# Kernel optimization log

Measured on AMD Instinct MI355X. Metric: run time of the kernel, lower is better.

Reference implementation:

```python
import jax, jax.numpy as jnp
import numpy as np

EPS = 1e-6
N_HEADS = 16


def _stable_softmax(x):
    # max subtracted with stop_gradient (torch .detach()), clamp to [-50, 50], eps in denom
    x_max = jax.lax.stop_gradient(jnp.max(x, axis=-1, keepdims=True))
    exp_x = jnp.exp(jnp.clip(x - x_max, -50.0, 50.0))
    return exp_x / (jnp.sum(exp_x, axis=-1, keepdims=True) + EPS)


def setup_inputs() -> dict:
    key = jax.random.key(0)
    k1, k2, k3 = jax.random.split(key, 3)
    B, S, D = 2, 2048, 1024
    x = jax.random.normal(k1, (B, S, D), dtype=jnp.float32)
    Wqkv = jax.random.normal(k2, (3 * D, D), dtype=jnp.float32) * 0.02
    Wout = jax.random.normal(k3, (D, D), dtype=jnp.float32) * (0.02 / np.sqrt(2))
    return {"x": x, "Wqkv": Wqkv, "Wout": Wout}


def reference(x, Wqkv, Wout):
    B, S, D = x.shape
    H = N_HEADS
    Dh = D // H
    scale = 1.0 / np.sqrt(Dh)
    # qkv projection (torch Linear: x @ W.T), split into q,k,v -> (B,H,S,Dh)
    qkv = (x @ Wqkv.T).reshape(B, S, 3, H, Dh)
    qkv = jnp.transpose(qkv, (2, 0, 3, 1, 4))
    q, k, v = qkv[0], qkv[1], qkv[2]
    # chunked attention is mathematically identical to full attention here
    scores = jnp.einsum('bhqd,bhkd->bhqk', q, k) * scale
    attn = _stable_softmax(scores)
    out = jnp.einsum('bhqk,bhkd->bhqd', attn, v)  # (B,H,S,Dh)
    out = jnp.transpose(out, (0, 2, 1, 3)).reshape(B, S, D)
    return out @ Wout.T
```

## Files before the change

### kernel.cpp

```cpp
#include <hip/hip_runtime.h>
#include <hip/hip_bf16.h>
#include <stdint.h>

#define S_LEN   2048
#define D_MODEL 1024
#define NH      16
#define DH      64
#define BATCH   2
#define TOKENS  (BATCH * S_LEN)

typedef __bf16 bf16;
typedef __bf16 bf16x8 __attribute__((ext_vector_type(8)));
typedef __bf16 b16x4  __attribute__((ext_vector_type(4)));
typedef short  s16x4  __attribute__((ext_vector_type(4)));
typedef float  f32x4  __attribute__((ext_vector_type(4)));

__device__ __forceinline__ void async_lds16(const void* g, void* l) {
  __builtin_amdgcn_global_load_lds((__attribute__((address_space(1))) void*)g,
                                   (__attribute__((address_space(3))) void*)l,
                                   16, 0, 0);
}

__global__ __launch_bounds__(256) void convert_kernel(
    const float* __restrict__ src, bf16* __restrict__ dst, int n8) {
  const int i = blockIdx.x * 256 + threadIdx.x;
  if (i >= n8) return;
  const f32x4 a = *(const f32x4*)(src + (size_t)i * 8);
  const f32x4 b = *(const f32x4*)(src + (size_t)i * 8 + 4);
  bf16x8 o;
#pragma unroll
  for (int j = 0; j < 4; j++) { o[j] = (bf16)a[j]; o[j + 4] = (bf16)b[j]; }
  *(bf16x8*)(dst + (size_t)i * 8) = o;
}

#define BM 128
#define BN 128
#define BK 32

#define GEMM_CORE(APTR, BPTR, KDIM)                                              \
  __shared__ __align__(16) bf16 As[BM * BK];                                     \
  __shared__ __align__(16) bf16 Bs[BN * BK];                                     \
  const int tid  = threadIdx.x;                                                  \
  const int wave = tid >> 6, lane = tid & 63;                                    \
  const int quad = lane >> 4, l16 = lane & 15;                                   \
  const int m0 = blockIdx.y * BM;                                                \
  const int n0 = blockIdx.x * BN;                                                \
  const int wm = (wave >> 1) * 64, wn = (wave & 1) * 64;                         \
  f32x4 acc[4][4] = {};                                                          \
  const int c0 = tid, c1 = tid + 256;                                            \
  for (int k0 = 0; k0 < (KDIM); k0 += BK) {                                      \
    async_lds16((APTR) + (size_t)(m0 + (c0 >> 2)) * (KDIM) + k0 + (c0 & 3) * 8,  \
                As + c0 * 8);                                                    \
    async_lds16((APTR) + (size_t)(m0 + (c1 >> 2)) * (KDIM) + k0 + (c1 & 3) * 8,  \
                As + c1 * 8);                                                    \
    async_lds16((BPTR) + (size_t)(n0 + (c0 >> 2)) * (KDIM) + k0 + (c0 & 3) * 8,  \
                Bs + c0 * 8);                                                    \
    async_lds16((BPTR) + (size_t)(n0 + (c1 >> 2)) * (KDIM) + k0 + (c1 & 3) * 8,  \
                Bs + c1 * 8);                                                    \
    __syncthreads();                                                             \
    bf16x8 af[4], bfr[4];                                                        \
    _Pragma("unroll") for (int i = 0; i < 4; i++)                                \
        af[i] = *(const bf16x8*)(As + (wm + i * 16 + l16) * BK + quad * 8);      \
    _Pragma("unroll") for (int j = 0; j < 4; j++)                                \
        bfr[j] = *(const bf16x8*)(Bs + (wn + j * 16 + l16) * BK + quad * 8);     \
    _Pragma("unroll") for (int i = 0; i < 4; i++)                                \
      _Pragma("unroll") for (int j = 0; j < 4; j++)                              \
        acc[i][j] = __builtin_amdgcn_mfma_f32_16x16x32_bf16(af[i], bfr[j],       \
                                                            acc[i][j], 0, 0, 0); \
    __syncthreads();                                                             \
  }

__global__ __launch_bounds__(256) void gemm_qkv_kernel(
    const bf16* __restrict__ X, const bf16* __restrict__ W,
    bf16* __restrict__ Qo, bf16* __restrict__ Ko, bf16* __restrict__ VTo) {
  GEMM_CORE(X, W, D_MODEL)
  const int t = n0 >> 10;
#pragma unroll
  for (int i = 0; i < 4; i++) {
    const int rowb = m0 + wm + i * 16 + quad * 4;
    const int b = rowb >> 11, s0 = rowb & 2047;
#pragma unroll
    for (int j = 0; j < 4; j++) {
      const int col = n0 + wn + j * 16 + l16;
      const int h = (col >> 6) & 15, d = col & 63;
      if (t == 2) {
        b16x4 v4;
#pragma unroll
        for (int r = 0; r < 4; r++) v4[r] = (bf16)acc[i][j][r];
        *(b16x4*)(VTo + ((size_t)(b * NH + h) * DH + d) * S_LEN + s0) = v4;
      } else {
#pragma unroll
        for (int r = 0; r < 4; r++) {
          const float v = acc[i][j][r];
          if (t == 0)
            Qo[((size_t)(b * NH + h) * S_LEN + s0 + r) * DH + d] = (bf16)(v * 0.125f);
          else
            Ko[((size_t)(b * NH + h) * S_LEN + s0 + r) * DH + d] = (bf16)v;
        }
      }
    }
  }
}

__global__ __launch_bounds__(256) void gemm_out_kernel(
    const bf16* __restrict__ A, const bf16* __restrict__ W,
    float* __restrict__ Out) {
  GEMM_CORE(A, W, D_MODEL)
#pragma unroll
  for (int i = 0; i < 4; i++) {
    const int rowb = m0 + wm + i * 16 + quad * 4;
#pragma unroll
    for (int j = 0; j < 4; j++) {
      const int col = n0 + wn + j * 16 + l16;
#pragma unroll
      for (int r = 0; r < 4; r++)
        Out[(size_t)(rowb + r) * D_MODEL + col] = acc[i][j][r];
    }
  }
}

#define AKS 72
#define AVS 72

__device__ __forceinline__ f32x4 mfma16(s16x4 a, s16x4 b, f32x4 c) {
  return __builtin_amdgcn_mfma_f32_16x16x16bf16_1k(a, b, c, 0, 0, 0);
}

__global__ __launch_bounds__(256) void attn_kernel(
    const bf16* __restrict__ Q, const bf16* __restrict__ K,
    const bf16* __restrict__ VT, bf16* __restrict__ AO) {
  __shared__ __align__(16) bf16 Ks[64 * AKS];
  __shared__ __align__(16) bf16 Vs[64 * AVS];

  const int tid  = threadIdx.x;
  const int wave = tid >> 6, lane = tid & 63;
  const int quad = lane >> 4, l16 = lane & 15;
  const int qb = blockIdx.x & 15;
  const int bh = blockIdx.x >> 4;
  const bf16* qp = Q  + (size_t)bh * S_LEN * DH;
  const bf16* kp = K  + (size_t)bh * S_LEN * DH;
  const bf16* vp = VT + (size_t)bh * DH * S_LEN;
  const int qr0 = qb * 128 + wave * 32;

  bf16x8 aq[2][2];
#pragma unroll
  for (int u = 0; u < 2; u++) {
    aq[u][0] = *(const bf16x8*)(qp + (size_t)(qr0 + u * 16 + l16) * DH + quad * 8);
    aq[u][1] = *(const bf16x8*)(qp + (size_t)(qr0 + u * 16 + l16) * DH + 32 + quad * 8);
  }

  f32x4 oT[2][4] = {};
  float lsum[2] = {0.f, 0.f};

  const int c0 = tid, c1 = tid + 256;
  const int r0c = c0 >> 3, r1c = c1 >> 3, k0c = (c0 & 7) * 8, k1c = (c1 & 7) * 8;

  for (int kb = 0; kb < S_LEN / 64; kb++) {
    const bf16x8 kv0 = *(const bf16x8*)(kp + (size_t)(kb * 64 + r0c) * DH + k0c);
    const bf16x8 kv1 = *(const bf16x8*)(kp + (size_t)(kb * 64 + r1c) * DH + k1c);
    const bf16x8 vv0 = *(const bf16x8*)(vp + (size_t)r0c * S_LEN + kb * 64 + k0c);
    const bf16x8 vv1 = *(const bf16x8*)(vp + (size_t)r1c * S_LEN + kb * 64 + k1c);
    __syncthreads();
    *(bf16x8*)(Ks + r0c * AKS + k0c) = kv0;
    *(bf16x8*)(Ks + r1c * AKS + k1c) = kv1;
    *(bf16x8*)(Vs + r0c * AVS + k0c) = vv0;
    *(bf16x8*)(Vs + r1c * AVS + k1c) = vv1;
    __syncthreads();

#pragma unroll
    for (int t = 0; t < 4; t++) {
      const bf16x8 ak0 = *(const bf16x8*)(Ks + (t * 16 + l16) * AKS + quad * 8);
      const bf16x8 ak1 = *(const bf16x8*)(Ks + (t * 16 + l16) * AKS + 32 + quad * 8);
      s16x4 av[4];
#pragma unroll
      for (int nt = 0; nt < 4; nt++)
        av[nt] = __builtin_bit_cast(
            s16x4, *(const b16x4*)(Vs + (nt * 16 + l16) * AVS + t * 16 + quad * 4));
#pragma unroll
      for (int u = 0; u < 2; u++) {
        f32x4 st = {};
        st = __builtin_amdgcn_mfma_f32_16x16x32_bf16(ak0, aq[u][0], st, 0, 0, 0);
        st = __builtin_amdgcn_mfma_f32_16x16x32_bf16(ak1, aq[u][1], st, 0, 0, 0);
        b16x4 pb;
#pragma unroll
        for (int r = 0; r < 4; r++) {
          pb[r] = (bf16)__expf(st[r]);
          lsum[u] += (float)pb[r];
        }
        const s16x4 pbs = __builtin_bit_cast(s16x4, pb);
#pragma unroll
        for (int nt = 0; nt < 4; nt++) oT[u][nt] = mfma16(av[nt], pbs, oT[u][nt]);
      }
    }
  }

#pragma unroll
  for (int u = 0; u < 2; u++) {
    float s = lsum[u];
    s += __shfl_xor(s, 16);
    s += __shfl_xor(s, 32);
    lsum[u] = s;
  }

  const int b = bh >> 4, h = bh & 15;
#pragma unroll
  for (int u = 0; u < 2; u++) {
    const float inv = 1.0f / (lsum[u] + 1e-6f);
    const int srow = qr0 + u * 16 + l16;
    const size_t base = (size_t)(b * S_LEN + srow) * D_MODEL + h * DH;
#pragma unroll
    for (int nt = 0; nt < 4; nt++) {
      b16x4 o4;
#pragma unroll
      for (int r = 0; r < 4; r++) o4[r] = (bf16)(oT[u][nt][r] * inv);
      *(b16x4*)(AO + base + nt * 16 + quad * 4) = o4;
    }
  }
}

extern "C" void kernel_launch(void* const* d_in, const int* in_sizes, int n_in,
                              void* d_out, int out_size, void* d_ws, size_t ws_size,
                              hipStream_t stream) {
  const float* x    = (const float*)d_in[0];
  const float* wqkv = (const float*)d_in[1];
  const float* wout = (const float*)d_in[2];
  float* out = (float*)d_out;

  bf16* Q  = (bf16*)d_ws;
  bf16* K  = Q  + (size_t)TOKENS * D_MODEL;
  bf16* VT = K  + (size_t)TOKENS * D_MODEL;
  bf16* xb = VT + (size_t)TOKENS * D_MODEL;
  bf16* AO = xb;
  bf16* wqkvb = (bf16*)d_out;
  bf16* woutb = Q;

  convert_kernel<<<dim3(TOKENS * D_MODEL / (256 * 8)), dim3(256), 0, stream>>>(
      x, xb, TOKENS * D_MODEL / 8);
  convert_kernel<<<dim3(3 * D_MODEL * D_MODEL / (256 * 8)), dim3(256), 0, stream>>>(
      wqkv, wqkvb, 3 * D_MODEL * D_MODEL / 8);

  gemm_qkv_kernel<<<dim3(3 * D_MODEL / BN, TOKENS / BM), dim3(256), 0, stream>>>(
      xb, wqkvb, Q, K, VT);

  attn_kernel<<<dim3(BATCH * NH * (S_LEN / 128)), dim3(256), 0, stream>>>(Q, K, VT, AO);

  convert_kernel<<<dim3(D_MODEL * D_MODEL / (256 * 8)), dim3(256), 0, stream>>>(
      wout, woutb, D_MODEL * D_MODEL / 8);

  gemm_out_kernel<<<dim3(D_MODEL / BN, TOKENS / BM), dim3(256), 0, stream>>>(
      AO, woutb, out);
}
```

Baseline: 206.2 us.

## Stage P through LDS to use 16x16x32 MFMA for PV and prefetch K/V

The attention kernel now writes the bf16 probability tiles to a per-wave LDS buffer so the P·V product can use the wider 16x16x32 bf16 MFMA instead of the 16x16x16 variant, halving the PV MFMA count. It also software-prefetches the next K/V tile into registers while the current tile is computed, hiding global load latency. The row sum is now accumulated from the fp32 exponentials rather than the rounded bf16 values. This adds LDS traffic, extra LDS use per block, and register pressure from the prefetched tiles.

```diff
diff --git a/kernel.cpp b/kernel.cpp
--- a/kernel.cpp
+++ b/kernel.cpp
@@ -12,7 +12,6 @@
 typedef __bf16 bf16;
 typedef __bf16 bf16x8 __attribute__((ext_vector_type(8)));
 typedef __bf16 b16x4  __attribute__((ext_vector_type(4)));
-typedef short  s16x4  __attribute__((ext_vector_type(4)));
 typedef float  f32x4  __attribute__((ext_vector_type(4)));
 
 __device__ __forceinline__ void async_lds16(const void* g, void* l) {
@@ -121,16 +120,14 @@
 
 #define AKS 72
 #define AVS 72
-
-__device__ __forceinline__ f32x4 mfma16(s16x4 a, s16x4 b, f32x4 c) {
-  return __builtin_amdgcn_mfma_f32_16x16x16bf16_1k(a, b, c, 0, 0, 0);
-}
+#define PTS 72
 
 __global__ __launch_bounds__(256) void attn_kernel(
     const bf16* __restrict__ Q, const bf16* __restrict__ K,
     const bf16* __restrict__ VT, bf16* __restrict__ AO) {
   __shared__ __align__(16) bf16 Ks[64 * AKS];
   __shared__ __align__(16) bf16 Vs[64 * AVS];
+  __shared__ __align__(16) bf16 PT[4 * 32 * PTS];
 
   const int tid  = threadIdx.x;
   const int wave = tid >> 6, lane = tid & 63;
@@ -151,15 +148,17 @@
 
   f32x4 oT[2][4] = {};
   float lsum[2] = {0.f, 0.f};
+  bf16* PTw = PT + wave * (32 * PTS);
 
   const int c0 = tid, c1 = tid + 256;
   const int r0c = c0 >> 3, r1c = c1 >> 3, k0c = (c0 & 7) * 8, k1c = (c1 & 7) * 8;
 
+  bf16x8 kv0 = *(const bf16x8*)(kp + (size_t)r0c * DH + k0c);
+  bf16x8 kv1 = *(const bf16x8*)(kp + (size_t)r1c * DH + k1c);
+  bf16x8 vv0 = *(const bf16x8*)(vp + (size_t)r0c * S_LEN + k0c);
+  bf16x8 vv1 = *(const bf16x8*)(vp + (size_t)r1c * S_LEN + k1c);
+
   for (int kb = 0; kb < S_LEN / 64; kb++) {
-    const bf16x8 kv0 = *(const bf16x8*)(kp + (size_t)(kb * 64 + r0c) * DH + k0c);
-    const bf16x8 kv1 = *(const bf16x8*)(kp + (size_t)(kb * 64 + r1c) * DH + k1c);
-    const bf16x8 vv0 = *(const bf16x8*)(vp + (size_t)r0c * S_LEN + kb * 64 + k0c);
-    const bf16x8 vv1 = *(const bf16x8*)(vp + (size_t)r1c * S_LEN + kb * 64 + k1c);
     __syncthreads();
     *(bf16x8*)(Ks + r0c * AKS + k0c) = kv0;
     *(bf16x8*)(Ks + r1c * AKS + k1c) = kv1;
@@ -167,29 +166,48 @@
     *(bf16x8*)(Vs + r1c * AVS + k1c) = vv1;
     __syncthreads();
 
+    const int kn = (kb + 1 < S_LEN / 64) ? kb + 1 : kb;
+    kv0 = *(const bf16x8*)(kp + (size_t)(kn * 64 + r0c) * DH + k0c);
+    kv1 = *(const bf16x8*)(kp + (size_t)(kn * 64 + r1c) * DH + k1c);
+    vv0 = *(const bf16x8*)(vp + (size_t)r0c * S_LEN + kn * 64 + k0c);
+    vv1 = *(const bf16x8*)(vp + (size_t)r1c * S_LEN + kn * 64 + k1c);
+
 #pragma unroll
     for (int t = 0; t < 4; t++) {
       const bf16x8 ak0 = *(const bf16x8*)(Ks + (t * 16 + l16) * AKS + quad * 8);
       const bf16x8 ak1 = *(const bf16x8*)(Ks + (t * 16 + l16) * AKS + 32 + quad * 8);
-      s16x4 av[4];
-#pragma unroll
-      for (int nt = 0; nt < 4; nt++)
-        av[nt] = __builtin_bit_cast(
-            s16x4, *(const b16x4*)(Vs + (nt * 16 + l16) * AVS + t * 16 + quad * 4));
 #pragma unroll
       for (int u = 0; u < 2; u++) {
         f32x4 st = {};
         st = __builtin_amdgcn_mfma_f32_16x16x32_bf16(ak0, aq[u][0], st, 0, 0, 0);
         st = __builtin_amdgcn_mfma_f32_16x16x32_bf16(ak1, aq[u][1], st, 0, 0, 0);
         b16x4 pb;
+        float ls = 0.f;
 #pragma unroll
         for (int r = 0; r < 4; r++) {
-          pb[r] = (bf16)__expf(st[r]);
-          lsum[u] += (float)pb[r];
+          const float e = __expf(st[r]);
+          ls += e;
+          pb[r] = (bf16)e;
         }
-        const s16x4 pbs = __builtin_bit_cast(s16x4, pb);
-#pragma unroll
-        for (int nt = 0; nt < 4; nt++) oT[u][nt] = mfma16(av[nt], pbs, oT[u][nt]);
+        lsum[u] += ls;
+        *(b16x4*)(PTw + (u * 16 + l16) * PTS + t * 16 + quad * 4) = pb;
+      }
+    }
+
+#pragma unroll
+    for (int c = 0; c < 2; c++) {
+      bf16x8 pf[2];
+#pragma unroll
+      for (int u = 0; u < 2; u++)
+        pf[u] = *(const bf16x8*)(PTw + (u * 16 + l16) * PTS + c * 32 + quad * 8);
+#pragma unroll
+      for (int nt = 0; nt < 4; nt++) {
+        const bf16x8 av =
+            *(const bf16x8*)(Vs + (nt * 16 + l16) * AVS + c * 32 + quad * 8);
+#pragma unroll
+        for (int u = 0; u < 2; u++)
+          oT[u][nt] = __builtin_amdgcn_mfma_f32_16x16x32_bf16(av, pf[u],
+                                                              oT[u][nt], 0, 0, 0);
       }
     }
   }
```

After: 205.7 us. No clear change (-0.2%).
